# Optimization experiments

Hardware: AMD Instinct MI355X
Metric: run time of the kernel (lower is better)

The kernel has to match this reference:

```python
import jax, jax.numpy as jnp
import numpy as np

B, N, D, P = 8, 64, 256, 256   # batch, nodes, input_features, proj_size_filler (== proj_size_role)
E = N * (N - 1)                # complete directed graph


def _layer_norm(x, g, b, eps=1e-5):
    mu = jnp.mean(x, axis=-1, keepdims=True)
    v = jnp.mean((x - mu) ** 2, axis=-1, keepdims=True)
    return (x - mu) * jax.lax.rsqrt(v + eps) * g + b


def _lin_init(k, fin, fout):
    k1, k2 = jax.random.split(k)
    lim = 1.0 / np.sqrt(fin)
    W = jax.random.uniform(k1, (fin, fout), minval=-lim, maxval=lim, dtype=jnp.float32)
    b = jax.random.uniform(k2, (fout,), minval=-lim, maxval=lim, dtype=jnp.float32)
    return W, b


def setup_inputs() -> dict:
    key = jax.random.key(0)
    ks = jax.random.split(key, 10)
    # complete directed graph, src-major order: node i -> all j != i
    src = np.repeat(np.arange(N), N - 1)
    mesh = np.tile(np.arange(N), (N, 1))
    dst = mesh[~np.eye(N, dtype=bool)].reshape(N, N - 1).ravel()
    edge_index = np.broadcast_to(np.stack([src, dst])[None], (B, 2, E)).copy()
    W_f0, b_f0 = _lin_init(ks[0], 3 * D, D)
    W_f1, b_f1 = _lin_init(ks[1], D, D)
    W_f2, b_f2 = _lin_init(ks[2], D, P)
    W_i0, b_i0 = _lin_init(ks[3], 2 * D + P, D)
    W_i1, b_i1 = _lin_init(ks[4], D, D)
    W_i2, b_i2 = _lin_init(ks[5], D, D)
    return {
        "node_features": jax.random.normal(ks[6], (B, N, D), dtype=jnp.float32),
        "edge_features": jax.random.normal(ks[7], (B, E, D), dtype=jnp.float32),
        "target_node": jax.random.normal(ks[8], (B, D), dtype=jnp.float32),
        "edge_index": jnp.asarray(edge_index, dtype=jnp.int32),
        "W_f0": W_f0, "b_f0": b_f0, "W_f1": W_f1, "b_f1": b_f1, "W_f2": W_f2, "b_f2": b_f2,
        "ln_gamma": jnp.ones((P,), jnp.float32), "ln_beta": jnp.zeros((P,), jnp.float32),
        "W_i0": W_i0, "b_i0": b_i0, "W_i1": W_i1, "b_i1": b_i1, "W_i2": W_i2, "b_i2": b_i2,
    }


def reference(node_features, edge_features, target_node, edge_index,
              W_f0, b_f0, W_f1, b_f1, W_f2, b_f2, ln_gamma, ln_beta,
              W_i0, b_i0, W_i1, b_i1, W_i2, b_i2):
    src = edge_index[:, 0, :]                                   # [B,E]
    dst = edge_index[:, 1, :]                                   # [B,E]
    nf_src = jnp.take_along_axis(node_features, src[..., None], axis=1)  # [B,E,D]
    nf_dst = jnp.take_along_axis(node_features, dst[..., None], axis=1)  # [B,E,D]
    # --- initialization: edge-wise MLP (original calls x.relu() without assignment ->
    # no activation; dropout is eval-mode identity) ---
    h = jnp.concatenate([nf_src, edge_features, nf_dst], axis=-1)        # [B,E,3D]
    h = h @ W_f0 + b_f0
    h = h @ W_f1 + b_f1
    filler = h @ W_f2 + b_f2                                             # [B,E,P]
    # scatter-add of per-edge outer products into node memory; edges are src-major
    # (node i owns edges i*(N-1):(i+1)*(N-1)) so the segment-sum is a block reshape.
    mem = jnp.einsum('bnep,bned->bnpd',
                     filler.reshape(B, N, N - 1, P),
                     nf_dst.reshape(B, N, N - 1, D))                     # [B,N,P,D]
    # --- propagation: complete graph => every pair adjacent => BFS yields only
    # trivial length-1 paths, which collect_long_dependancy ignores (identity). ---
    # --- inference ---
    retrieved = jnp.einsum('bnpd,bd->bnp', mem, target_node)             # [B,N,P]
    retrieved = _layer_norm(retrieved, ln_gamma, ln_beta)
    tgt = jnp.broadcast_to(target_node[:, None, :], (B, N, D))
    z = jnp.concatenate([node_features, retrieved, tgt], axis=-1)        # [B,N,2D+P]
    z = z @ W_i0 + b_i0
    z = z @ W_i1 + b_i1
    z = z @ W_i2 + b_i2                                                  # [B,N,D]
    return z
```

## Files before the change

### kernel.cpp

```cpp
#include <hip/hip_runtime.h>

#define BB 8
#define NN 64
#define DD 256
#define PP 256
#define NE 63
#define EE 4032

typedef _Float16 half4 __attribute__((ext_vector_type(4)));
typedef _Float16 half2v __attribute__((ext_vector_type(2)));

__global__ __launch_bounds__(256) void k_wconv(const float* __restrict__ Wf0, const float* __restrict__ Wf1,
                                               const float* __restrict__ Wf2, const float* __restrict__ Wi0,
                                               const float* __restrict__ Wi1, const float* __restrict__ Wi2,
                                               _Float16* __restrict__ o) {
    int i = (blockIdx.x * 256 + threadIdx.x) * 2;
    const float* src; int off;
    if (i < 196608)      { src = Wf0; off = 0; }
    else if (i < 262144) { src = Wf1; off = 196608; }
    else if (i < 327680) { src = Wf2; off = 262144; }
    else if (i < 524288) { src = Wi0; off = 327680; }
    else if (i < 589824) { src = Wi1; off = 524288; }
    else                 { src = Wi2; off = 589824; }
    float2 v = *(const float2*)(src + (i - off));
    half2v h; h.x = (_Float16)v.x; h.y = (_Float16)v.y;
    *(half2v*)(o + i) = h;
}

__global__ __launch_bounds__(64) void k_dot(const float* __restrict__ nf,
                                            const float* __restrict__ tgt,
                                            float* __restrict__ dotv) {
    int row = blockIdx.x;
    int b = row >> 6;
    int lane = threadIdx.x;
    const float4* x4 = (const float4*)(nf + (size_t)row * DD);
    const float4* t4 = (const float4*)(tgt + (size_t)b * DD);
    float4 a = x4[lane];
    float4 c = t4[lane];
    float acc = a.x * c.x + a.y * c.y + a.z * c.z + a.w * c.w;
#pragma unroll
    for (int off = 32; off; off >>= 1) acc += __shfl_down(acc, off, 64);
    if (lane == 0) dotv[row] = acc;
}

__global__ __launch_bounds__(1024) void k_edge(const float* __restrict__ nf,
                                               const float* __restrict__ ef,
                                               const int* __restrict__ eidx,
                                               const float* __restrict__ dotv,
                                               float* __restrict__ conc,
                                               float* __restrict__ Svec) {
    __shared__ float s_sh[64];
    __shared__ int src_sh[NE];
    __shared__ int dst_sh[NE];
    __shared__ float Psh[16 * 768];
    int bn = blockIdx.x;
    int b = bn >> 6, n = bn & 63;
    int tid = threadIdx.x;
    int lane = tid & 63;
    int h = tid >> 6;

    if (tid < NE) {
        const int* srcp = eidx + (size_t)b * 2 * EE + n * NE;
        int si = srcp[tid];
        int di = srcp[EE + tid];
        src_sh[tid] = si;
        dst_sh[tid] = di;
        s_sh[tid] = dotv[(b << 6) + di];
    }
    __syncthreads();

    if (tid < 64) {
        float v = (tid < NE) ? s_sh[tid] : 0.f;
#pragma unroll
        for (int off = 32; off; off >>= 1) v += __shfl_down(v, off, 64);
        if (tid == 0) Svec[bn] = v;
    }

    const float4* nf4 = (const float4*)nf;
    const float4* ef4 = (const float4*)ef;
    size_t efbase = ((size_t)b * EE + (size_t)n * NE) * 64 + lane;
    size_t nfbase = (size_t)(b << 6) * 64 + lane;
    int e0 = h * 4, e1 = min(NE, h * 4 + 4);
    float4 at = {0,0,0,0}, aus = {0,0,0,0}, aud = {0,0,0,0};
#pragma unroll 4
    for (int e = e0; e < e1; ++e) {
        float sv = s_sh[e];
        float4 fe = ef4[efbase + (size_t)e * 64];
        float4 fs = nf4[nfbase + (size_t)src_sh[e] * 64];
        float4 fd = nf4[nfbase + (size_t)dst_sh[e] * 64];
        at.x += sv * fe.x; at.y += sv * fe.y; at.z += sv * fe.z; at.w += sv * fe.w;
        aus.x += sv * fs.x; aus.y += sv * fs.y; aus.z += sv * fs.z; aus.w += sv * fs.w;
        aud.x += sv * fd.x; aud.y += sv * fd.y; aud.z += sv * fd.z; aud.w += sv * fd.w;
    }
    float4* Pf4 = (float4*)Psh;
    Pf4[(size_t)(h * 3 + 0) * 64 + lane] = aus;
    Pf4[(size_t)(h * 3 + 1) * 64 + lane] = at;
    Pf4[(size_t)(h * 3 + 2) * 64 + lane] = aud;
    __syncthreads();

    if (tid < 768) {
        float s = 0.f;
#pragma unroll
        for (int hh = 0; hh < 16; ++hh) s += Psh[hh * 768 + tid];
        conc[(size_t)bn * 768 + tid] = s;
    }
}

__global__ __launch_bounds__(1024) void k_mlp(const float* __restrict__ conc,
                                              const float* __restrict__ Svec,
                                              const float* __restrict__ nf,
                                              const float* __restrict__ tgt,
                                              const _Float16* __restrict__ Wh,
                                              const float* __restrict__ bf0,
                                              const float* __restrict__ bf1,
                                              const float* __restrict__ bf2,
                                              const float* __restrict__ gam, const float* __restrict__ bet,
                                              const float* __restrict__ bi0,
                                              const float* __restrict__ bi1,
                                              const float* __restrict__ bi2,
                                              float* __restrict__ outp) {
    __shared__ float At[768 * 4];
    __shared__ float Zt[768 * 4];
    __shared__ float P[16 * 4 * 256];
    __shared__ float Ht[256 * 4];
    __shared__ float red1[16], red2[16];
    int r0 = blockIdx.x * 4;
    int tid = threadIdx.x;
    int jg = tid & 63;
    int h = tid >> 6;
    int col = tid & 255;
    int r2 = tid >> 8;

    const _Float16* Wf0h = Wh;
    const _Float16* Wf1h = Wh + 196608;
    const _Float16* Wf2h = Wh + 262144;
    const _Float16* Wi0h = Wh + 327680;
    const _Float16* Wi1h = Wh + 524288;
    const _Float16* Wi2h = Wh + 589824;

    {
        const float* cp = conc + (size_t)(r0 + r2) * 768;
#pragma unroll
        for (int q = 0; q < 3; ++q) {
            int k = col + q * 256;
            At[k * 4 + r2] = cp[k];
        }
        Zt[col * 4 + r2]         = nf[(size_t)(r0 + r2) * DD + col];
        Zt[(512 + col) * 4 + r2] = tgt[(size_t)((r0 + r2) >> 6) * DD + col];
    }
    float Sv = Svec[r0 + r2];
    __syncthreads();

    auto layer = [&](const float* Xt, int K, const _Float16* __restrict__ W,
                     const float* __restrict__ bias, bool scaleS,
                     float* OUTt, bool store) -> float {
        int kpart = K >> 4;
        const half4* Wp = (const half4*)(W + (size_t)(h * kpart) * 256) + jg;
        const float4* Xp = (const float4*)Xt + h * kpart;
        float4 a0 = {0,0,0,0}, a1 = {0,0,0,0}, a2 = {0,0,0,0}, a3 = {0,0,0,0};
#pragma unroll 8
        for (int k = 0; k < kpart; ++k) {
            half4 wh = Wp[(size_t)k * 64];
            float4 x = Xp[k];
            float wx = (float)wh.x, wy = (float)wh.y, wz = (float)wh.z, ww = (float)wh.w;
            a0.x += x.x * wx; a0.y += x.x * wy; a0.z += x.x * wz; a0.w += x.x * ww;
            a1.x += x.y * wx; a1.y += x.y * wy; a1.z += x.y * wz; a1.w += x.y * ww;
            a2.x += x.z * wx; a2.y += x.z * wy; a2.z += x.z * wz; a2.w += x.z * ww;
            a3.x += x.w * wx; a3.y += x.w * wy; a3.z += x.w * wz; a3.w += x.w * ww;
        }
        float4* Pf4 = (float4*)P;
        Pf4[(size_t)(h * 4 + 0) * 64 + jg] = a0;
        Pf4[(size_t)(h * 4 + 1) * 64 + jg] = a1;
        Pf4[(size_t)(h * 4 + 2) * 64 + jg] = a2;
        Pf4[(size_t)(h * 4 + 3) * 64 + jg] = a3;
        __syncthreads();
        float v = 0.f;
#pragma unroll
        for (int hh = 0; hh < 16; ++hh) v += P[(hh * 4 + r2) * 256 + col];
        v += (scaleS ? Sv : 1.f) * bias[col];
        if (store) {
            OUTt[col * 4 + r2] = v;
        }
        __syncthreads();
        return v;
    };

    layer(At, 768, Wf0h, bf0, true, Ht, true);
    layer(Ht, 256, Wf1h, bf1, true, Ht, true);
    float v = layer(Ht, 256, Wf2h, bf2, true, nullptr, false);

    {
        float s1 = v, s2 = v * v;
#pragma unroll
        for (int off = 32; off; off >>= 1) {
            s1 += __shfl_down(s1, off, 64);
            s2 += __shfl_down(s2, off, 64);
        }
        int wv = (tid >> 6) & 3;
        if ((tid & 63) == 0) { red1[r2 * 4 + wv] = s1; red2[r2 * 4 + wv] = s2; }
        __syncthreads();
        float sum = red1[r2 * 4] + red1[r2 * 4 + 1] + red1[r2 * 4 + 2] + red1[r2 * 4 + 3];
        float sq  = red2[r2 * 4] + red2[r2 * 4 + 1] + red2[r2 * 4 + 2] + red2[r2 * 4 + 3];
        float mu  = sum * (1.f / 256.f);
        float var = sq * (1.f / 256.f) - mu * mu;
        float inv = rsqrtf(var + 1e-5f);
        Zt[(256 + col) * 4 + r2] = (v - mu) * inv * gam[col] + bet[col];
        __syncthreads();
    }

    layer(Zt, 768, Wi0h, bi0, false, Ht, true);
    layer(Ht, 256, Wi1h, bi1, false, Ht, true);
    float o = layer(Ht, 256, Wi2h, bi2, false, nullptr, false);
    outp[(size_t)(r0 + r2) * 256 + col] = o;
}

extern "C" void kernel_launch(void* const* d_in, const int* in_sizes, int n_in,
                              void* d_out, int out_size, void* d_ws, size_t ws_size,
                              hipStream_t stream) {
    const float* nf  = (const float*)d_in[0];
    const float* ef  = (const float*)d_in[1];
    const float* tgt = (const float*)d_in[2];
    const int*   ei  = (const int*)d_in[3];
    const float* Wf0 = (const float*)d_in[4];
    const float* bf0 = (const float*)d_in[5];
    const float* Wf1 = (const float*)d_in[6];
    const float* bf1 = (const float*)d_in[7];
    const float* Wf2 = (const float*)d_in[8];
    const float* bf2 = (const float*)d_in[9];
    const float* gam = (const float*)d_in[10];
    const float* bet = (const float*)d_in[11];
    const float* Wi0 = (const float*)d_in[12];
    const float* bi0 = (const float*)d_in[13];
    const float* Wi1 = (const float*)d_in[14];
    const float* bi1 = (const float*)d_in[15];
    const float* Wi2 = (const float*)d_in[16];
    const float* bi2 = (const float*)d_in[17];
    float* out = (float*)d_out;

    float* dotv = (float*)d_ws;
    float* Svec = dotv + 512;
    float* conc = Svec + 512;
    _Float16* wh = (_Float16*)(conc + 512 * 768);

    k_wconv<<<655360 / 512, 256, 0, stream>>>(Wf0, Wf1, Wf2, Wi0, Wi1, Wi2, wh);
    k_dot<<<BB * NN, 64, 0, stream>>>(nf, tgt, dotv);
    k_edge<<<BB * NN, 1024, 0, stream>>>(nf, ef, ei, dotv, conc, Svec);
    k_mlp<<<(BB * NN) / 4, 1024, 0, stream>>>(conc, Svec, nf, tgt, wh,
                                              bf0, bf1, bf2, gam, bet,
                                              bi0, bi1, bi2, out);
}
```

Before: 143.6 us.

## Fuse weight conversion and dot-product kernels into the edge kernel

Merges the three front kernels (fp32-to-fp16 weight conversion, per-node dot with the target, and the per-edge reduction) into one k_front launch. Each block converts a 1280-element slice of the weights and recomputes the dot products it needs locally with wave reductions, instead of reading a precomputed dotv buffer. This removes two kernel launches and one global round trip. In exchange, dot products are computed redundantly across blocks and an extra block-wide sync is added before the edge loop.

```diff
diff --git a/kernel.cpp b/kernel.cpp
--- a/kernel.cpp
+++ b/kernel.cpp
@@ -10,45 +10,16 @@
 typedef _Float16 half4 __attribute__((ext_vector_type(4)));
 typedef _Float16 half2v __attribute__((ext_vector_type(2)));
 
-__global__ __launch_bounds__(256) void k_wconv(const float* __restrict__ Wf0, const float* __restrict__ Wf1,
-                                               const float* __restrict__ Wf2, const float* __restrict__ Wi0,
-                                               const float* __restrict__ Wi1, const float* __restrict__ Wi2,
-                                               _Float16* __restrict__ o) {
-    int i = (blockIdx.x * 256 + threadIdx.x) * 2;
-    const float* src; int off;
-    if (i < 196608)      { src = Wf0; off = 0; }
-    else if (i < 262144) { src = Wf1; off = 196608; }
-    else if (i < 327680) { src = Wf2; off = 262144; }
-    else if (i < 524288) { src = Wi0; off = 327680; }
-    else if (i < 589824) { src = Wi1; off = 524288; }
-    else                 { src = Wi2; off = 589824; }
-    float2 v = *(const float2*)(src + (i - off));
-    half2v h; h.x = (_Float16)v.x; h.y = (_Float16)v.y;
-    *(half2v*)(o + i) = h;
-}
-
-__global__ __launch_bounds__(64) void k_dot(const float* __restrict__ nf,
-                                            const float* __restrict__ tgt,
-                                            float* __restrict__ dotv) {
-    int row = blockIdx.x;
-    int b = row >> 6;
-    int lane = threadIdx.x;
-    const float4* x4 = (const float4*)(nf + (size_t)row * DD);
-    const float4* t4 = (const float4*)(tgt + (size_t)b * DD);
-    float4 a = x4[lane];
-    float4 c = t4[lane];
-    float acc = a.x * c.x + a.y * c.y + a.z * c.z + a.w * c.w;
-#pragma unroll
-    for (int off = 32; off; off >>= 1) acc += __shfl_down(acc, off, 64);
-    if (lane == 0) dotv[row] = acc;
-}
-
-__global__ __launch_bounds__(1024) void k_edge(const float* __restrict__ nf,
-                                               const float* __restrict__ ef,
-                                               const int* __restrict__ eidx,
-                                               const float* __restrict__ dotv,
-                                               float* __restrict__ conc,
-                                               float* __restrict__ Svec) {
+__global__ __launch_bounds__(1024) void k_front(const float* __restrict__ nf,
+                                                const float* __restrict__ ef,
+                                                const int* __restrict__ eidx,
+                                                const float* __restrict__ tgt,
+                                                const float* __restrict__ Wf0, const float* __restrict__ Wf1,
+                                                const float* __restrict__ Wf2, const float* __restrict__ Wi0,
+                                                const float* __restrict__ Wi1, const float* __restrict__ Wi2,
+                                                _Float16* __restrict__ wh,
+                                                float* __restrict__ conc,
+                                                float* __restrict__ Svec) {
     __shared__ float s_sh[64];
     __shared__ int src_sh[NE];
     __shared__ int dst_sh[NE];
@@ -59,13 +30,39 @@
     int lane = tid & 63;
     int h = tid >> 6;
 
+    if (tid < 640) {
+        int i = bn * 1280 + tid * 2;
+        const float* src; int off;
+        if (i < 196608)      { src = Wf0; off = 0; }
+        else if (i < 262144) { src = Wf1; off = 196608; }
+        else if (i < 327680) { src = Wf2; off = 262144; }
+        else if (i < 524288) { src = Wi0; off = 327680; }
+        else if (i < 589824) { src = Wi1; off = 524288; }
+        else                 { src = Wi2; off = 589824; }
+        float2 v = *(const float2*)(src + (i - off));
+        half2v hh; hh.x = (_Float16)v.x; hh.y = (_Float16)v.y;
+        *(half2v*)(wh + i) = hh;
+    }
+
     if (tid < NE) {
         const int* srcp = eidx + (size_t)b * 2 * EE + n * NE;
-        int si = srcp[tid];
-        int di = srcp[EE + tid];
-        src_sh[tid] = si;
-        dst_sh[tid] = di;
-        s_sh[tid] = dotv[(b << 6) + di];
+        src_sh[tid] = srcp[tid];
+        dst_sh[tid] = srcp[EE + tid];
+    }
+    __syncthreads();
+
+    const float4* nf4  = (const float4*)nf;
+    const float4* tgt4 = (const float4*)(tgt + (size_t)b * DD);
+    float4 c4 = tgt4[lane];
+
+    int e0 = h * 4, e1 = min(NE, h * 4 + 4);
+    for (int e = e0; e < e1; ++e) {
+        int d = dst_sh[e];
+        float4 a4 = nf4[(size_t)((b << 6) + d) * 64 + lane];
+        float p = a4.x * c4.x + a4.y * c4.y + a4.z * c4.z + a4.w * c4.w;
+#pragma unroll
+        for (int off = 32; off; off >>= 1) p += __shfl_down(p, off, 64);
+        if (lane == 0) s_sh[e] = p;
     }
     __syncthreads();
 
@@ -76,11 +73,9 @@
         if (tid == 0) Svec[bn] = v;
     }
 
-    const float4* nf4 = (const float4*)nf;
     const float4* ef4 = (const float4*)ef;
     size_t efbase = ((size_t)b * EE + (size_t)n * NE) * 64 + lane;
     size_t nfbase = (size_t)(b << 6) * 64 + lane;
-    int e0 = h * 4, e1 = min(NE, h * 4 + 4);
     float4 at = {0,0,0,0}, aus = {0,0,0,0}, aud = {0,0,0,0};
 #pragma unroll 4
     for (int e = e0; e < e1; ++e) {
@@ -160,9 +155,9 @@
         float4 a0 = {0,0,0,0}, a1 = {0,0,0,0}, a2 = {0,0,0,0}, a3 = {0,0,0,0};
 #pragma unroll 8
         for (int k = 0; k < kpart; ++k) {
-            half4 wh = Wp[(size_t)k * 64];
+            half4 wh4 = Wp[(size_t)k * 64];
             float4 x = Xp[k];
-            float wx = (float)wh.x, wy = (float)wh.y, wz = (float)wh.z, ww = (float)wh.w;
+            float wx = (float)wh4.x, wy = (float)wh4.y, wz = (float)wh4.z, ww = (float)wh4.w;
             a0.x += x.x * wx; a0.y += x.x * wy; a0.z += x.x * wz; a0.w += x.x * ww;
             a1.x += x.y * wx; a1.y += x.y * wy; a1.z += x.y * wz; a1.w += x.y * ww;
             a2.x += x.z * wx; a2.y += x.z * wy; a2.z += x.z * wz; a2.w += x.z * ww;
@@ -237,14 +232,13 @@
     const float* bi2 = (const float*)d_in[17];
     float* out = (float*)d_out;
 
-    float* dotv = (float*)d_ws;
-    float* Svec = dotv + 512;
+    float* Svec = (float*)d_ws;
     float* conc = Svec + 512;
     _Float16* wh = (_Float16*)(conc + 512 * 768);
 
-    k_wconv<<<655360 / 512, 256, 0, stream>>>(Wf0, Wf1, Wf2, Wi0, Wi1, Wi2, wh);
-    k_dot<<<BB * NN, 64, 0, stream>>>(nf, tgt, dotv);
-    k_edge<<<BB * NN, 1024, 0, stream>>>(nf, ef, ei, dotv, conc, Svec);
+    k_front<<<BB * NN, 1024, 0, stream>>>(nf, ef, ei, tgt,
+                                          Wf0, Wf1, Wf2, Wi0, Wi1, Wi2,
+                                          wh, conc, Svec);
     k_mlp<<<(BB * NN) / 4, 1024, 0, stream>>>(conc, Svec, nf, tgt, wh,
                                               bf0, bf1, bf2, gam, bet,
                                               bi0, bi1, bi2, out);
```

After: 143.7 us. No clear change (+0.0%).
